# Optimization experiments

Measured on AMD Instinct MI355X. Metric: run time of the kernel, lower is better.

## Reference

```python
import jax, jax.numpy as jnp
import numpy as np

B, S, H, A, C = 2, 128, 1024, 256, 14


def setup_inputs() -> dict:
    key = jax.random.key(0)
    ks = jax.random.split(key, 20)
    def p(k, shape, scale=0.02):
        return jax.random.normal(k, shape, dtype=jnp.float32) * scale
    inp = {"memory": jax.random.normal(ks[0], (B, S, H), dtype=jnp.float32)}
    i = 1
    for name in ("h", "t", "m"):
        inp[f"{name}_W1"] = p(ks[i], (H, A)); i += 1
        inp[f"{name}_b1"] = jnp.zeros((A,), jnp.float32)
        inp[f"{name}_W2"] = p(ks[i], (A, A)); i += 1
        inp[f"{name}_b2"] = jnp.zeros((A,), jnp.float32)
        inp[f"s0{name}_W"] = p(ks[i], (A, C)); i += 1
        inp[f"s0{name}_b"] = jnp.zeros((C,), jnp.float32)
        inp[f"s1{name}_W"] = p(ks[i], (A, C)); i += 1
        inp[f"s1{name}_b"] = jnp.zeros((C,), jnp.float32)
    inp["uni"] = jax.random.normal(ks[i], (C,), dtype=jnp.float32)
    return inp


def _mlp(x, W1, b1, W2, b2):
    # 2-layer MLP (Linear -> ReLU -> Linear), dropout=0 / eval mode
    return jax.nn.relu(x @ W1 + b1) @ W2 + b2


def reference(memory,
              h_W1, h_b1, h_W2, h_b2, s0h_W, s0h_b, s1h_W, s1h_b,
              t_W1, t_b1, t_W2, t_b2, s0t_W, s0t_b, s1t_W, s1t_b,
              m_W1, m_b1, m_W2, m_b2, s0m_W, s0m_b, s1m_W, s1m_b,
              uni):
    seq = memory.shape[1]
    head = _mlp(memory, h_W1, h_b1, h_W2, h_b2)   # [B,S,A]
    tail = _mlp(memory, t_W1, t_b1, t_W2, t_b2)
    mid = _mlp(memory, m_W1, m_b1, m_W2, m_b2)

    sh0 = head @ s0h_W + s0h_b   # [B,S,C]
    st0 = tail @ s0t_W + s0t_b
    sm0 = mid @ s0m_W + s0m_b
    # score[b,i,j,k,c] = sh0[b,i,c] + st0[b,j,c] + sm0[b,k,c]
    score = sh0[:, :, None, None, :] + st0[:, None, :, None, :] + sm0[:, None, None, :, :]

    idx = jnp.arange(seq)
    # mask where k > j or k < i (mid index must lie in [head, tail])
    bad = (idx[None, None, :] > idx[None, :, None]) | (idx[None, None, :] < idx[:, None, None])  # [S,S,S]
    score = jnp.where(bad[None, :, :, :, None], jnp.float32(-1e6), score)

    alpha = jax.nn.softmax(score, axis=3)  # softmax over mid index k

    sh1 = head @ s1h_W + s1h_b  # note: original uses head/tail/mid (not head1) for score1
    st1 = tail @ s1t_W + s1t_b
    sm1 = mid @ s1m_W + s1m_b
    score1 = sh1[:, :, None, None, :] + st1[:, None, :, None, :] + sm1[:, None, None, :, :]

    final_score = jnp.sum(alpha * score1, axis=3) + uni[None, None, None, :]  # [B,S,S,C]
    return final_score
```

## Files before the change

### kernel.cpp

```cpp
#include <hip/hip_runtime.h>

#define BB 2
#define SS 128
#define HH 1024
#define AA 256
#define CC 14
#define R_TOT (BB*SS)

struct NetP { const float *W1,*b1,*W2,*b2,*s0W,*s0b,*s1W,*s1b; };
struct AllP { NetP n[3]; };

#define S0_OFF 0
#define S1_OFF (3*R_TOT*CC)
#define HID_OFF 32768

__global__ __launch_bounds__(512)
void hid_kernel(const float* __restrict__ mem, AllP P, float* __restrict__ hid)
{
    const int bx  = blockIdx.x;
    const int net = bx >> 7;
    const int rem = bx & 127;
    const int rt  = rem >> 2;
    const int ct  = rem & 3;
    const int row0 = rt * 8;
    const int lane = threadIdx.x & 63;
    const int wv   = __builtin_amdgcn_readfirstlane(threadIdx.x >> 6);
    const int col  = ct*64 + lane;
    const NetP p = P.n[net];

    __shared__ float part[8][8][64];

    float acc[8] = {0,0,0,0,0,0,0,0};
    const int k0 = wv * 128;
    const float* __restrict__ W1p  = p.W1 + (size_t)k0*AA + col;
    const float* __restrict__ memp = mem + (size_t)row0*HH + k0;
    #pragma unroll 8
    for (int kk = 0; kk < 128; ++kk) {
        const float w = W1p[(size_t)kk*AA];
        #pragma unroll
        for (int r = 0; r < 8; ++r)
            acc[r] = fmaf(memp[(size_t)r*HH + kk], w, acc[r]);
    }
    #pragma unroll
    for (int r = 0; r < 8; ++r) part[wv][r][lane] = acc[r];
    __syncthreads();

    const int r = threadIdx.x >> 6;
    const int l = threadIdx.x & 63;
    float s = p.b1[ct*64 + l];
    #pragma unroll
    for (int w = 0; w < 8; ++w) s += part[w][r][l];
    hid[((size_t)net*R_TOT + row0 + r)*AA + ct*64 + l] = fmaxf(s, 0.f);
}

__global__ __launch_bounds__(512)
void out_kernel(const float* __restrict__ hid, AllP P,
                float* __restrict__ s0o, float* __restrict__ s1o)
{
    const int bx  = blockIdx.x;
    const int net = bx >> 6;
    const int rt  = bx & 63;
    const int row0 = rt * 4;
    const NetP p = P.n[net];
    const int col = threadIdx.x & 255;
    const int kh  = __builtin_amdgcn_readfirstlane(threadIdx.x >> 8);

    __shared__ float part[2][4][256];
    __shared__ float outp[4][256];
    __shared__ float pp[112][4];

    const float* __restrict__ hb = hid + ((size_t)net*R_TOT + row0)*AA;
    float acc[4] = {0,0,0,0};
    const int k0 = kh * 128;
    const float* __restrict__ W2p = p.W2 + (size_t)k0*AA + col;
    #pragma unroll 8
    for (int kk = 0; kk < 128; ++kk) {
        const float w = W2p[(size_t)kk*AA];
        #pragma unroll
        for (int r = 0; r < 4; ++r)
            acc[r] = fmaf(hb[(size_t)r*AA + k0 + kk], w, acc[r]);
    }
    #pragma unroll
    for (int r = 0; r < 4; ++r) part[kh][r][col] = acc[r];
    __syncthreads();

    for (int i = threadIdx.x; i < 4*AA; i += 512) {
        const int r = i >> 8, u = i & 255;
        outp[r][u] = part[0][r][u] + part[1][r][u] + p.b2[u];
    }
    __syncthreads();

    const int t = threadIdx.x;
    if (t < 448) {
        const int task = t >> 2, kc = t & 3;
        const int which = (task >= 56) ? 1 : 0;
        const int rem2  = task - which*56;
        const int rr = rem2 / CC, c = rem2 % CC;
        const float* __restrict__ W = which ? p.s1W : p.s0W;
        float s = 0.f;
        #pragma unroll 4
        for (int k = kc*64; k < kc*64 + 64; ++k)
            s = fmaf(outp[rr][k], W[(size_t)k*CC + c], s);
        pp[task][kc] = s;
    }
    __syncthreads();
    if (t < 112) {
        const int which = (t >= 56) ? 1 : 0;
        const int rem2  = t - which*56;
        const int rr = rem2 / CC, c = rem2 % CC;
        const float s = pp[t][0]+pp[t][1]+pp[t][2]+pp[t][3] + (which ? p.s1b : p.s0b)[c];
        (which ? s1o : s0o)[((size_t)net*R_TOT + row0 + rr)*CC + c] = s;
    }
}

__global__ __launch_bounds__(512)
void final_kernel(const float* __restrict__ s0w, const float* __restrict__ s1w,
                  const float* __restrict__ uni, float* __restrict__ out)
{
    const int bi = blockIdx.x;
    const int b = bi >> 7, i = bi & (SS-1);
    const int tid = threadIdx.x;
    const int lane = tid & 63;
    const int k    = tid & 127;
    const int wv2  = (tid >> 6) & 1;
    const int slot = tid >> 7;

    __shared__ float E[SS*CC];
    __shared__ float Qe[SS*CC];
    __shared__ float red[4][4][2];
    __shared__ float mnL[CC], sh1L[CC], uniL[CC];

    if (tid < CC) {
        sh1L[tid] = s1w[(size_t)bi*CC + tid];
        uniL[tid] = uni[tid];
    }

    const float* __restrict__ sm0b = s0w + (size_t)(2*R_TOT + b*SS)*CC;
    const float* __restrict__ sm1b = s1w + (size_t)(2*R_TOT + b*SS)*CC;

    for (int pass = 0; pass < 4; ++pass) {
        const int c = pass*4 + slot;
        float x0 = 0.f, x1 = 0.f, e = 0.f, q = 0.f;
        if (c < CC) {
            x0 = sm0b[(size_t)k*CC + c];
            x1 = sm1b[(size_t)k*CC + c];
            float m = x0;
            #pragma unroll
            for (int off = 32; off >= 1; off >>= 1) m = fmaxf(m, __shfl_xor(m, off));
            float ss = x1;
            #pragma unroll
            for (int off = 32; off >= 1; off >>= 1) ss += __shfl_xor(ss, off);
            if (lane == 0) { red[0][slot][wv2] = m; red[1][slot][wv2] = ss; }
        }
        __syncthreads();
        if (c < CC) {
            const float M = fmaxf(red[0][slot][0], red[0][slot][1]);
            e = __expf(x0 - M);
            q = e * x1;
            #pragma unroll
            for (int off = 1; off <= 32; off <<= 1) {
                const float te = __shfl_up(e, off);
                const float tq = __shfl_up(q, off);
                if (lane >= off) { e += te; q += tq; }
            }
            if (lane == 63) { red[2][slot][wv2] = e; red[3][slot][wv2] = q; }
        }
        __syncthreads();
        if (c < CC) {
            if (wv2 == 1) { e += red[2][slot][0]; q += red[3][slot][0]; }
            E [k*CC + c] = e;
            Qe[k*CC + c] = q;
            if (k == 0) mnL[c] = (red[1][slot][0] + red[1][slot][1]) * (1.f/SS);
        }
        __syncthreads();
    }

    const float* __restrict__ st1 = s1w + (size_t)(R_TOT + b*SS)*CC;
    float* __restrict__ o = out + (size_t)bi*SS*CC;
    if (tid < 448) {
        const int e0 = tid * 4;
        float v[4];
        #pragma unroll
        for (int u = 0; u < 4; ++u) {
            const int idx = e0 + u;
            const int j = idx / CC, c = idx - j*CC;
            float add;
            if (i <= j) {
                const float Ei = (i > 0) ? E [(i-1)*CC + c] : 0.f;
                const float Qi = (i > 0) ? Qe[(i-1)*CC + c] : 0.f;
                add = (Qe[j*CC + c] - Qi) / (E[j*CC + c] - Ei);
            } else {
                add = mnL[c];
            }
            v[u] = sh1L[c] + st1[idx] + uniL[c] + add;
        }
        *(float4*)&o[e0] = make_float4(v[0], v[1], v[2], v[3]);
    }
}

extern "C" void kernel_launch(void* const* d_in, const int* in_sizes, int n_in,
                              void* d_out, int out_size, void* d_ws, size_t ws_size,
                              hipStream_t stream)
{
    const float* mem = (const float*)d_in[0];
    AllP P;
    for (int n = 0; n < 3; ++n) {
        const int base = 1 + 8*n;
        P.n[n].W1  = (const float*)d_in[base+0];
        P.n[n].b1  = (const float*)d_in[base+1];
        P.n[n].W2  = (const float*)d_in[base+2];
        P.n[n].b2  = (const float*)d_in[base+3];
        P.n[n].s0W = (const float*)d_in[base+4];
        P.n[n].s0b = (const float*)d_in[base+5];
        P.n[n].s1W = (const float*)d_in[base+6];
        P.n[n].s1b = (const float*)d_in[base+7];
    }
    const float* uni = (const float*)d_in[25];
    float* ws  = (float*)d_ws;
    float* s0  = ws + S0_OFF;
    float* s1  = ws + S1_OFF;
    float* hid = ws + HID_OFF;
    float* out = (float*)d_out;

    hipLaunchKernelGGL(hid_kernel,   dim3(384),    dim3(512), 0, stream, mem, P, hid);
    hipLaunchKernelGGL(out_kernel,   dim3(192),    dim3(512), 0, stream, hid, P, s0, s1);
    hipLaunchKernelGGL(final_kernel, dim3(BB*SS),  dim3(512), 0, stream, s0, s1, uni, out);
}
```

Baseline: 33.16 us.

## Fuse both MLP layers and score projections into one kernel

Merges hid_kernel and out_kernel into a single kernel in which each block computes 4 rows across all 256 hidden columns. The hidden activations stay in shared memory rather than going through global workspace, and one launch is removed. Each thread now computes 4 columns for 4 rows using float4 weight loads. The cost is fewer blocks (192 instead of 384 for the first GEMM) and more work per block, which may reduce parallelism for the W1 stage.

```diff
diff --git a/kernel.cpp b/kernel.cpp
--- a/kernel.cpp
+++ b/kernel.cpp
@@ -12,87 +12,98 @@
 
 #define S0_OFF 0
 #define S1_OFF (3*R_TOT*CC)
-#define HID_OFF 32768
 
 __global__ __launch_bounds__(512)
-void hid_kernel(const float* __restrict__ mem, AllP P, float* __restrict__ hid)
+void mlp_fused(const float* __restrict__ mem, AllP P,
+               float* __restrict__ s0o, float* __restrict__ s1o)
 {
-    const int bx  = blockIdx.x;
-    const int net = bx >> 7;
-    const int rem = bx & 127;
-    const int rt  = rem >> 2;
-    const int ct  = rem & 3;
-    const int row0 = rt * 8;
-    const int lane = threadIdx.x & 63;
-    const int wv   = __builtin_amdgcn_readfirstlane(threadIdx.x >> 6);
-    const int col  = ct*64 + lane;
-    const NetP p = P.n[net];
-
-    __shared__ float part[8][8][64];
-
-    float acc[8] = {0,0,0,0,0,0,0,0};
-    const int k0 = wv * 128;
-    const float* __restrict__ W1p  = p.W1 + (size_t)k0*AA + col;
-    const float* __restrict__ memp = mem + (size_t)row0*HH + k0;
-    #pragma unroll 8
-    for (int kk = 0; kk < 128; ++kk) {
-        const float w = W1p[(size_t)kk*AA];
+    const int bx   = blockIdx.x;
+    const int net  = bx >> 6;
+    const int rt   = bx & 63;
+    const int row0 = rt * 4;
+    const NetP p  = P.n[net];
+    const int tid  = threadIdx.x;
+    const int lane = tid & 63;
+    const int wv   = __builtin_amdgcn_readfirstlane(tid >> 6);
+    const int col4 = 4 * lane;
+
+    __shared__ float part[8][4][AA];
+    __shared__ float hidL[4][AA];
+    __shared__ float outL[4][AA];
+    __shared__ float pp[112][4];
+
+    {
+        const int k0 = wv * 128;
+        const float* __restrict__ W1p = p.W1 + (size_t)k0*AA + col4;
+        const float* __restrict__ m0 = mem + (size_t)(row0+0)*HH + k0;
+        const float* __restrict__ m1 = mem + (size_t)(row0+1)*HH + k0;
+        const float* __restrict__ m2 = mem + (size_t)(row0+2)*HH + k0;
+        const float* __restrict__ m3 = mem + (size_t)(row0+3)*HH + k0;
+        float4 a0 = {0,0,0,0}, a1 = {0,0,0,0}, a2 = {0,0,0,0}, a3 = {0,0,0,0};
+        #pragma unroll 4
+        for (int kk = 0; kk < 128; ++kk) {
+            const float4 w4 = *(const float4*)(W1p + (size_t)kk*AA);
+            const float v0 = m0[kk], v1 = m1[kk], v2 = m2[kk], v3 = m3[kk];
+            a0.x = fmaf(v0, w4.x, a0.x); a0.y = fmaf(v0, w4.y, a0.y);
+            a0.z = fmaf(v0, w4.z, a0.z); a0.w = fmaf(v0, w4.w, a0.w);
+            a1.x = fmaf(v1, w4.x, a1.x); a1.y = fmaf(v1, w4.y, a1.y);
+            a1.z = fmaf(v1, w4.z, a1.z); a1.w = fmaf(v1, w4.w, a1.w);
+            a2.x = fmaf(v2, w4.x, a2.x); a2.y = fmaf(v2, w4.y, a2.y);
+            a2.z = fmaf(v2, w4.z, a2.z); a2.w = fmaf(v2, w4.w, a2.w);
+            a3.x = fmaf(v3, w4.x, a3.x); a3.y = fmaf(v3, w4.y, a3.y);
+            a3.z = fmaf(v3, w4.z, a3.z); a3.w = fmaf(v3, w4.w, a3.w);
+        }
+        *(float4*)&part[wv][0][col4] = a0;
+        *(float4*)&part[wv][1][col4] = a1;
+        *(float4*)&part[wv][2][col4] = a2;
+        *(float4*)&part[wv][3][col4] = a3;
+    }
+    __syncthreads();
+    for (int i = tid; i < 4*AA; i += 512) {
+        const int r = i >> 8, u = i & (AA-1);
+        float s = p.b1[u];
         #pragma unroll
-        for (int r = 0; r < 8; ++r)
-            acc[r] = fmaf(memp[(size_t)r*HH + kk], w, acc[r]);
-    }
-    #pragma unroll
-    for (int r = 0; r < 8; ++r) part[wv][r][lane] = acc[r];
-    __syncthreads();
-
-    const int r = threadIdx.x >> 6;
-    const int l = threadIdx.x & 63;
-    float s = p.b1[ct*64 + l];
-    #pragma unroll
-    for (int w = 0; w < 8; ++w) s += part[w][r][l];
-    hid[((size_t)net*R_TOT + row0 + r)*AA + ct*64 + l] = fmaxf(s, 0.f);
-}
-
-__global__ __launch_bounds__(512)
-void out_kernel(const float* __restrict__ hid, AllP P,
-                float* __restrict__ s0o, float* __restrict__ s1o)
-{
-    const int bx  = blockIdx.x;
-    const int net = bx >> 6;
-    const int rt  = bx & 63;
-    const int row0 = rt * 4;
-    const NetP p = P.n[net];
-    const int col = threadIdx.x & 255;
-    const int kh  = __builtin_amdgcn_readfirstlane(threadIdx.x >> 8);
-
-    __shared__ float part[2][4][256];
-    __shared__ float outp[4][256];
-    __shared__ float pp[112][4];
-
-    const float* __restrict__ hb = hid + ((size_t)net*R_TOT + row0)*AA;
-    float acc[4] = {0,0,0,0};
-    const int k0 = kh * 128;
-    const float* __restrict__ W2p = p.W2 + (size_t)k0*AA + col;
-    #pragma unroll 8
-    for (int kk = 0; kk < 128; ++kk) {
-        const float w = W2p[(size_t)kk*AA];
+        for (int w = 0; w < 8; ++w) s += part[w][r][u];
+        hidL[r][u] = fmaxf(s, 0.f);
+    }
+    __syncthreads();
+
+    {
+        const int k0 = wv * 32;
+        const float* __restrict__ W2p = p.W2 + (size_t)k0*AA + col4;
+        float4 a0 = {0,0,0,0}, a1 = {0,0,0,0}, a2 = {0,0,0,0}, a3 = {0,0,0,0};
+        #pragma unroll 4
+        for (int kk = 0; kk < 32; ++kk) {
+            const float4 w4 = *(const float4*)(W2p + (size_t)kk*AA);
+            const float v0 = hidL[0][k0+kk], v1 = hidL[1][k0+kk];
+            const float v2 = hidL[2][k0+kk], v3 = hidL[3][k0+kk];
+            a0.x = fmaf(v0, w4.x, a0.x); a0.y = fmaf(v0, w4.y, a0.y);
+            a0.z = fmaf(v0, w4.z, a0.z); a0.w = fmaf(v0, w4.w, a0.w);
+            a1.x = fmaf(v1, w4.x, a1.x); a1.y = fmaf(v1, w4.y, a1.y);
+            a1.z = fmaf(v1, w4.z, a1.z); a1.w = fmaf(v1, w4.w, a1.w);
+            a2.x = fmaf(v2, w4.x, a2.x); a2.y = fmaf(v2, w4.y, a2.y);
+            a2.z = fmaf(v2, w4.z, a2.z); a2.w = fmaf(v2, w4.w, a2.w);
+            a3.x = fmaf(v3, w4.x, a3.x); a3.y = fmaf(v3, w4.y, a3.y);
+            a3.z = fmaf(v3, w4.z, a3.z); a3.w = fmaf(v3, w4.w, a3.w);
+        }
+        __syncthreads();
+        *(float4*)&part[wv][0][col4] = a0;
+        *(float4*)&part[wv][1][col4] = a1;
+        *(float4*)&part[wv][2][col4] = a2;
+        *(float4*)&part[wv][3][col4] = a3;
+    }
+    __syncthreads();
+    for (int i = tid; i < 4*AA; i += 512) {
+        const int r = i >> 8, u = i & (AA-1);
+        float s = p.b2[u];
         #pragma unroll
-        for (int r = 0; r < 4; ++r)
-            acc[r] = fmaf(hb[(size_t)r*AA + k0 + kk], w, acc[r]);
-    }
-    #pragma unroll
-    for (int r = 0; r < 4; ++r) part[kh][r][col] = acc[r];
-    __syncthreads();
-
-    for (int i = threadIdx.x; i < 4*AA; i += 512) {
-        const int r = i >> 8, u = i & 255;
-        outp[r][u] = part[0][r][u] + part[1][r][u] + p.b2[u];
-    }
-    __syncthreads();
-
-    const int t = threadIdx.x;
-    if (t < 448) {
-        const int task = t >> 2, kc = t & 3;
+        for (int w = 0; w < 8; ++w) s += part[w][r][u];
+        outL[r][u] = s;
+    }
+    __syncthreads();
+
+    if (tid < 448) {
+        const int task = tid >> 2, kc = tid & 3;
         const int which = (task >= 56) ? 1 : 0;
         const int rem2  = task - which*56;
         const int rr = rem2 / CC, c = rem2 % CC;
@@ -100,15 +111,16 @@
         float s = 0.f;
         #pragma unroll 4
         for (int k = kc*64; k < kc*64 + 64; ++k)
-            s = fmaf(outp[rr][k], W[(size_t)k*CC + c], s);
+            s = fmaf(outL[rr][k], W[(size_t)k*CC + c], s);
         pp[task][kc] = s;
     }
     __syncthreads();
-    if (t < 112) {
-        const int which = (t >= 56) ? 1 : 0;
-        const int rem2  = t - which*56;
+    if (tid < 112) {
+        const int which = (tid >= 56) ? 1 : 0;
+        const int rem2  = tid - which*56;
         const int rr = rem2 / CC, c = rem2 % CC;
-        const float s = pp[t][0]+pp[t][1]+pp[t][2]+pp[t][3] + (which ? p.s1b : p.s0b)[c];
+        const float s = pp[tid][0]+pp[tid][1]+pp[tid][2]+pp[tid][3]
+                      + (which ? p.s1b : p.s0b)[c];
         (which ? s1o : s0o)[((size_t)net*R_TOT + row0 + rr)*CC + c] = s;
     }
 }
@@ -219,10 +231,8 @@
     float* ws  = (float*)d_ws;
     float* s0  = ws + S0_OFF;
     float* s1  = ws + S1_OFF;
-    float* hid = ws + HID_OFF;
     float* out = (float*)d_out;
 
-    hipLaunchKernelGGL(hid_kernel,   dim3(384),    dim3(512), 0, stream, mem, P, hid);
-    hipLaunchKernelGGL(out_kernel,   dim3(192),    dim3(512), 0, stream, hid, P, s0, s1);
-    hipLaunchKernelGGL(final_kernel, dim3(BB*SS),  dim3(512), 0, stream, s0, s1, uni, out);
+    hipLaunchKernelGGL(mlp_fused,    dim3(192),   dim3(512), 0, stream, mem, P, s0, s1);
+    hipLaunchKernelGGL(final_kernel, dim3(BB*SS), dim3(512), 0, stream, s0, s1, uni, out);
 }
```

Result: faster. 31.09 us (-6.3%).

## Replace scalar FP32 MLP GEMMs with bf16 MFMA kernels and split-K reduction

Applied to the files above, without the earlier changes.

Adds a conversion kernel that casts memory and the transposed W1/W2 weights to bf16. The two MLP layers are replaced with MFMA 16x16x32 bf16 GEMMs: layer 1 uses split-K partials and a separate reduce kernel that applies bias and ReLU, and layer 2 is a direct GEMM. The small C=14 projections move into their own kernel. This trades FP32 scalar FMA work for matrix cores, but adds three extra launches, a per-call weight conversion, very low block counts (24 and 6), and reduced precision.

```diff
diff --git a/kernel.cpp b/kernel.cpp
--- a/kernel.cpp
+++ b/kernel.cpp
@@ -1,4 +1,5 @@
 #include <hip/hip_runtime.h>
+#include <hip/hip_bf16.h>
 
 #define BB 2
 #define SS 128
@@ -7,109 +8,245 @@
 #define CC 14
 #define R_TOT (BB*SS)
 
+typedef float  f32x4   __attribute__((ext_vector_type(4)));
+typedef short  short8  __attribute__((ext_vector_type(8)));
+typedef unsigned short ushort8v __attribute__((ext_vector_type(8)));
+
 struct NetP { const float *W1,*b1,*W2,*b2,*s0W,*s0b,*s1W,*s1b; };
 struct AllP { NetP n[3]; };
 
-#define S0_OFF 0
-#define S1_OFF (3*R_TOT*CC)
-#define HID_OFF 32768
+#define OFF_S0   0
+#define OFF_S1   43008
+#define OFF_P1   86016
+#define OFF_HIDB 3231744
+#define OFF_OUT2 3624960
+#define OFF_MEMB 4411392
+#define OFF_W1T  4935680
+#define OFF_W2T  6508544
+
+__device__ __forceinline__ unsigned short f2b(float x) {
+    return __bfloat16_as_ushort(__float2bfloat16(x));
+}
+
+__global__ __launch_bounds__(256)
+void cvt_kernel(const float* __restrict__ mem, AllP P,
+                unsigned short* __restrict__ membf,
+                unsigned short* __restrict__ w1t,
+                unsigned short* __restrict__ w2t)
+{
+    __shared__ float t[64][65];
+    const int bx = blockIdx.x, tid = threadIdx.x;
+    if (bx < 240) {
+        const bool isW1 = bx < 192;
+        const int idx  = isW1 ? bx : bx - 192;
+        const int net  = isW1 ? (idx >> 6) : (idx >> 4);
+        const int tile = isW1 ? (idx & 63) : (idx & 15);
+        const int kt = tile >> 2, nt = tile & 3;
+        const int k0 = kt*64, n0 = nt*64;
+        const float* __restrict__ W = isW1 ? P.n[net].W1 : P.n[net].W2;
+        #pragma unroll
+        for (int p = 0; p < 4; ++p) {
+            const int row = p*16 + (tid >> 4);
+            const int col = (tid & 15) * 4;
+            const float4 v = *(const float4*)(W + (size_t)(k0+row)*AA + n0 + col);
+            t[row][col] = v.x; t[row][col+1] = v.y;
+            t[row][col+2] = v.z; t[row][col+3] = v.w;
+        }
+        __syncthreads();
+        unsigned short* __restrict__ out =
+            isW1 ? (w1t + (size_t)net*AA*HH) : (w2t + (size_t)net*AA*AA);
+        const int ldout = isW1 ? HH : AA;
+        #pragma unroll
+        for (int p = 0; p < 2; ++p) {
+            const int nr = p*32 + (tid >> 3);
+            const int kg = (tid & 7) * 8;
+            ushort8v o;
+            #pragma unroll
+            for (int j = 0; j < 8; ++j) o[j] = f2b(t[kg + j][nr]);
+            *(ushort8v*)(out + (size_t)(n0 + nr)*ldout + k0 + kg) = o;
+        }
+    } else {
+        const int f = (bx - 240) * 2048 + tid * 8;
+        const float4 v0 = *(const float4*)(mem + f);
+        const float4 v1 = *(const float4*)(mem + f + 4);
+        ushort8v o;
+        o[0]=f2b(v0.x); o[1]=f2b(v0.y); o[2]=f2b(v0.z); o[3]=f2b(v0.w);
+        o[4]=f2b(v1.x); o[5]=f2b(v1.y); o[6]=f2b(v1.z); o[7]=f2b(v1.w);
+        *(ushort8v*)(membf + f) = o;
+    }
+}
 
 __global__ __launch_bounds__(512)
-void hid_kernel(const float* __restrict__ mem, AllP P, float* __restrict__ hid)
-{
-    const int bx  = blockIdx.x;
-    const int net = bx >> 7;
-    const int rem = bx & 127;
-    const int rt  = rem >> 2;
-    const int ct  = rem & 3;
-    const int row0 = rt * 8;
-    const int lane = threadIdx.x & 63;
-    const int wv   = __builtin_amdgcn_readfirstlane(threadIdx.x >> 6);
-    const int col  = ct*64 + lane;
-    const NetP p = P.n[net];
-
-    __shared__ float part[8][8][64];
-
-    float acc[8] = {0,0,0,0,0,0,0,0};
-    const int k0 = wv * 128;
-    const float* __restrict__ W1p  = p.W1 + (size_t)k0*AA + col;
-    const float* __restrict__ memp = mem + (size_t)row0*HH + k0;
-    #pragma unroll 8
-    for (int kk = 0; kk < 128; ++kk) {
-        const float w = W1p[(size_t)kk*AA];
-        #pragma unroll
-        for (int r = 0; r < 8; ++r)
-            acc[r] = fmaf(memp[(size_t)r*HH + kk], w, acc[r]);
-    }
-    #pragma unroll
-    for (int r = 0; r < 8; ++r) part[wv][r][lane] = acc[r];
+void gemm1_kernel(const unsigned short* __restrict__ membf,
+                  const unsigned short* __restrict__ w1t,
+                  float* __restrict__ p1)
+{
+    const int net = blockIdx.x >> 3;
+    const int nh  = (blockIdx.x >> 2) & 1;
+    const int kc  = blockIdx.x & 3;
+    const int tid = threadIdx.x, lane = tid & 63;
+    const int wv  = tid >> 6;
+    const int wm  = wv >> 1, wn = wv & 1;
+    const int lrow = lane & 15;
+    const int lk   = (lane >> 4) * 8;
+
+    const unsigned short* __restrict__ Ab =
+        membf + (size_t)(wm*64 + lrow)*HH + kc*256 + lk;
+    const unsigned short* __restrict__ Bb =
+        w1t + (size_t)net*AA*HH + (size_t)(nh*128 + wn*64 + lrow)*HH + kc*256 + lk;
+
+    f32x4 acc[4][4];
+    #pragma unroll
+    for (int i = 0; i < 4; ++i)
+        #pragma unroll
+        for (int j = 0; j < 4; ++j) acc[i][j] = (f32x4){0.f,0.f,0.f,0.f};
+
+    #pragma unroll 2
+    for (int ks = 0; ks < 8; ++ks) {
+        short8 a[4], b[4];
+        #pragma unroll
+        for (int f = 0; f < 4; ++f) {
+            a[f] = *(const short8*)(Ab + (size_t)f*16*HH + ks*32);
+            b[f] = *(const short8*)(Bb + (size_t)f*16*HH + ks*32);
+        }
+        #pragma unroll
+        for (int fm = 0; fm < 4; ++fm)
+            #pragma unroll
+            for (int fn = 0; fn < 4; ++fn)
+                acc[fm][fn] = __builtin_amdgcn_mfma_f32_16x16x32_bf16(
+                    a[fm], b[fn], acc[fm][fn], 0, 0, 0);
+    }
+
+    float* __restrict__ Pt = p1 + (size_t)blockIdx.x * (256*128);
+    const int drow = (lane >> 4) * 4;
+    const int dcol = lane & 15;
+    #pragma unroll
+    for (int fm = 0; fm < 4; ++fm)
+        #pragma unroll
+        for (int fn = 0; fn < 4; ++fn) {
+            const int m = wm*64 + fm*16 + drow;
+            const int n = wn*64 + fn*16 + dcol;
+            #pragma unroll
+            for (int r = 0; r < 4; ++r)
+                Pt[(size_t)(m + r)*128 + n] = acc[fm][fn][r];
+        }
+}
+
+__global__ __launch_bounds__(256)
+void reduce1_kernel(const float* __restrict__ p1, AllP P,
+                    unsigned short* __restrict__ hidb)
+{
+    const int net = blockIdx.x >> 5;
+    const int nh  = (blockIdx.x >> 4) & 1;
+    const int mt  = blockIdx.x & 15;
+    const int tid = threadIdx.x;
+    const int row = mt*16 + (tid >> 4);
+    const int n8  = (tid & 15) * 8;
+    const float* __restrict__ base =
+        p1 + (size_t)((net*2 + nh)*4) * (256*128) + (size_t)row*128 + n8;
+    float s[8] = {0,0,0,0,0,0,0,0};
+    #pragma unroll
+    for (int kcv = 0; kcv < 4; ++kcv) {
+        const float4 u0 = *(const float4*)(base + (size_t)kcv*(256*128));
+        const float4 u1 = *(const float4*)(base + (size_t)kcv*(256*128) + 4);
+        s[0]+=u0.x; s[1]+=u0.y; s[2]+=u0.z; s[3]+=u0.w;
+        s[4]+=u1.x; s[5]+=u1.y; s[6]+=u1.z; s[7]+=u1.w;
+    }
+    const float* __restrict__ b1 = P.n[net].b1 + nh*128 + n8;
+    ushort8v o;
+    #pragma unroll
+    for (int j = 0; j < 8; ++j) o[j] = f2b(fmaxf(s[j] + b1[j], 0.f));
+    *(ushort8v*)(hidb + (size_t)net*AA*AA + (size_t)row*AA + nh*128 + n8) = o;
+}
+
+__global__ __launch_bounds__(512)
+void gemm2_kernel(const unsigned short* __restrict__ hidb,
+                  const unsigned short* __restrict__ w2t, AllP P,
+                  float* __restrict__ out2)
+{
+    const int net = blockIdx.x >> 1;
+    const int nh  = blockIdx.x & 1;
+    const int tid = threadIdx.x, lane = tid & 63;
+    const int wv  = tid >> 6;
+    const int wm  = wv >> 1, wn = wv & 1;
+    const int lrow = lane & 15;
+    const int lk   = (lane >> 4) * 8;
+
+    const unsigned short* __restrict__ Ab =
+        hidb + (size_t)net*AA*AA + (size_t)(wm*64 + lrow)*AA + lk;
+    const unsigned short* __restrict__ Bb =
+        w2t + (size_t)net*AA*AA + (size_t)(nh*128 + wn*64 + lrow)*AA + lk;
+
+    f32x4 acc[4][4];
+    #pragma unroll
+    for (int i = 0; i < 4; ++i)
+        #pragma unroll
+        for (int j = 0; j < 4; ++j) acc[i][j] = (f32x4){0.f,0.f,0.f,0.f};
+
+    #pragma unroll 2
+    for (int ks = 0; ks < 8; ++ks) {
+        short8 a[4], b[4];
+        #pragma unroll
+        for (int f = 0; f < 4; ++f) {
+            a[f] = *(const short8*)(Ab + (size_t)f*16*AA + ks*32);
+            b[f] = *(const short8*)(Bb + (size_t)f*16*AA + ks*32);
+        }
+        #pragma unroll
+        for (int fm = 0; fm < 4; ++fm)
+            #pragma unroll
+            for (int fn = 0; fn < 4; ++fn)
+                acc[fm][fn] = __builtin_amdgcn_mfma_f32_16x16x32_bf16(
+                    a[fm], b[fn], acc[fm][fn], 0, 0, 0);
+    }
+
+    float* __restrict__ O = out2 + (size_t)net*AA*AA;
+    const float* __restrict__ b2 = P.n[net].b2;
+    const int drow = (lane >> 4) * 4;
+    const int dcol = lane & 15;
+    #pragma unroll
+    for (int fm = 0; fm < 4; ++fm)
+        #pragma unroll
+        for (int fn = 0; fn < 4; ++fn) {
+            const int m = wm*64 + fm*16 + drow;
+            const int n = nh*128 + wn*64 + fn*16 + dcol;
+            const float bv = b2[n];
+            #pragma unroll
+            for (int r = 0; r < 4; ++r)
+                O[(size_t)(m + r)*AA + n] = acc[fm][fn][r] + bv;
+        }
+}
+
+__global__ __launch_bounds__(512)
+void proj_kernel(const float* __restrict__ out2, AllP P,
+                 float* __restrict__ s0o, float* __restrict__ s1o)
+{
+    const int net  = blockIdx.x >> 4;
+    const int rt   = blockIdx.x & 15;
+    const int row0 = rt * 16;
+    const int tid  = threadIdx.x;
+    __shared__ float ldsT[256][16];
+    #pragma unroll
+    for (int u = 0; u < 2; ++u) {
+        const int idx = tid*8 + u*4;
+        const int row = idx >> 8;
+        const int k   = idx & 255;
+        const float4 v = *(const float4*)(out2 + (size_t)net*AA*AA
+                                          + (size_t)(row0+row)*AA + k);
+        ldsT[k][row] = v.x; ldsT[k+1][row] = v.y;
+        ldsT[k+2][row] = v.z; ldsT[k+3][row] = v.w;
+    }
     __syncthreads();
-
-    const int r = threadIdx.x >> 6;
-    const int l = threadIdx.x & 63;
-    float s = p.b1[ct*64 + l];
-    #pragma unroll
-    for (int w = 0; w < 8; ++w) s += part[w][r][l];
-    hid[((size_t)net*R_TOT + row0 + r)*AA + ct*64 + l] = fmaxf(s, 0.f);
-}
-
-__global__ __launch_bounds__(512)
-void out_kernel(const float* __restrict__ hid, AllP P,
-                float* __restrict__ s0o, float* __restrict__ s1o)
-{
-    const int bx  = blockIdx.x;
-    const int net = bx >> 6;
-    const int rt  = bx & 63;
-    const int row0 = rt * 4;
-    const NetP p = P.n[net];
-    const int col = threadIdx.x & 255;
-    const int kh  = __builtin_amdgcn_readfirstlane(threadIdx.x >> 8);
-
-    __shared__ float part[2][4][256];
-    __shared__ float outp[4][256];
-    __shared__ float pp[112][4];
-
-    const float* __restrict__ hb = hid + ((size_t)net*R_TOT + row0)*AA;
-    float acc[4] = {0,0,0,0};
-    const int k0 = kh * 128;
-    const float* __restrict__ W2p = p.W2 + (size_t)k0*AA + col;
-    #pragma unroll 8
-    for (int kk = 0; kk < 128; ++kk) {
-        const float w = W2p[(size_t)kk*AA];
-        #pragma unroll
-        for (int r = 0; r < 4; ++r)
-            acc[r] = fmaf(hb[(size_t)r*AA + k0 + kk], w, acc[r]);
-    }
-    #pragma unroll
-    for (int r = 0; r < 4; ++r) part[kh][r][col] = acc[r];
-    __syncthreads();
-
-    for (int i = threadIdx.x; i < 4*AA; i += 512) {
-        const int r = i >> 8, u = i & 255;
-        outp[r][u] = part[0][r][u] + part[1][r][u] + p.b2[u];
-    }
-    __syncthreads();
-
-    const int t = threadIdx.x;
-    if (t < 448) {
-        const int task = t >> 2, kc = t & 3;
-        const int which = (task >= 56) ? 1 : 0;
-        const int rem2  = task - which*56;
-        const int rr = rem2 / CC, c = rem2 % CC;
+    if (tid < 448) {
+        const int which = (tid >= 224) ? 1 : 0;
+        const int rem = tid - which*224;
+        const int r = rem / CC, c = rem % CC;
+        const NetP p = P.n[net];
         const float* __restrict__ W = which ? p.s1W : p.s0W;
-        float s = 0.f;
+        float s = (which ? p.s1b : p.s0b)[c];
         #pragma unroll 4
-        for (int k = kc*64; k < kc*64 + 64; ++k)
-            s = fmaf(outp[rr][k], W[(size_t)k*CC + c], s);
-        pp[task][kc] = s;
-    }
-    __syncthreads();
-    if (t < 112) {
-        const int which = (t >= 56) ? 1 : 0;
-        const int rem2  = t - which*56;
-        const int rr = rem2 / CC, c = rem2 % CC;
-        const float s = pp[t][0]+pp[t][1]+pp[t][2]+pp[t][3] + (which ? p.s1b : p.s0b)[c];
-        (which ? s1o : s0o)[((size_t)net*R_TOT + row0 + rr)*CC + c] = s;
+        for (int k = 0; k < AA; ++k)
+            s = fmaf(ldsT[k][r], W[(size_t)k*CC + c], s);
+        (which ? s1o : s0o)[((size_t)net*R_TOT + row0 + r)*CC + c] = s;
     }
 }
 
@@ -216,13 +353,21 @@
         P.n[n].s1b = (const float*)d_in[base+7];
     }
     const float* uni = (const float*)d_in[25];
-    float* ws  = (float*)d_ws;
-    float* s0  = ws + S0_OFF;
-    float* s1  = ws + S1_OFF;
-    float* hid = ws + HID_OFF;
+    char* wsb = (char*)d_ws;
+    float* s0   = (float*)(wsb + OFF_S0);
+    float* s1   = (float*)(wsb + OFF_S1);
+    float* p1   = (float*)(wsb + OFF_P1);
+    float* out2 = (float*)(wsb + OFF_OUT2);
+    unsigned short* hidb  = (unsigned short*)(wsb + OFF_HIDB);
+    unsigned short* membf = (unsigned short*)(wsb + OFF_MEMB);
+    unsigned short* w1t   = (unsigned short*)(wsb + OFF_W1T);
+    unsigned short* w2t   = (unsigned short*)(wsb + OFF_W2T);
     float* out = (float*)d_out;
 
-    hipLaunchKernelGGL(hid_kernel,   dim3(384),    dim3(512), 0, stream, mem, P, hid);
-    hipLaunchKernelGGL(out_kernel,   dim3(192),    dim3(512), 0, stream, hid, P, s0, s1);
-    hipLaunchKernelGGL(final_kernel, dim3(BB*SS),  dim3(512), 0, stream, s0, s1, uni, out);
-}
+    hipLaunchKernelGGL(cvt_kernel,     dim3(368), dim3(256), 0, stream, mem, P, membf, w1t, w2t);
+    hipLaunchKernelGGL(gemm1_kernel,   dim3(24),  dim3(512), 0, stream, membf, w1t, p1);
+    hipLaunchKernelGGL(reduce1_kernel, dim3(96),  dim3(256), 0, stream, p1, P, hidb);
+    hipLaunchKernelGGL(gemm2_kernel,   dim3(6),   dim3(512), 0, stream, hidb, w2t, P, out2);
+    hipLaunchKernelGGL(proj_kernel,    dim3(48),  dim3(512), 0, stream, out2, P, s0, s1);
+    hipLaunchKernelGGL(final_kernel,   dim3(BB*SS), dim3(512), 0, stream, s0, s1, uni, out);
+}
```

New measurement: 67.26 us. 2.03x slower.
